# Kernel tuning notes

Measured on AMD Instinct MI355X. Metric: run time of the kernel, lower is better.

The kernel has to match this reference:

```python
import jax, jax.numpy as jnp
import numpy as np

N_NODES = 50000
N_EDGES = 800000
NFEAT, NHID, NCLASS, NCLUSTER = 512, 64, 16, 32


def gcn_conv(x, W, b, edge_index, edge_weight, n):
    """PyG GCNConv: add self-loops, symmetric normalization, linear + scatter-add."""
    row, col = edge_index[0], edge_index[1]
    loop = jnp.arange(n, dtype=row.dtype)
    row = jnp.concatenate([row, loop])
    col = jnp.concatenate([col, loop])
    w = jnp.concatenate([edge_weight, jnp.ones((n,), dtype=edge_weight.dtype)])
    # degree computed on target index (gcn_norm convention)
    deg = jax.ops.segment_sum(w, col, num_segments=n)
    dinv = jnp.where(deg > 0, jax.lax.rsqrt(deg), 0.0)
    norm = dinv[row] * w * dinv[col]          # [E+n]
    xw = x @ W                                # [n, out]
    msg = xw[row] * norm[:, None]             # gather + scale
    out = jax.ops.segment_sum(msg, col, num_segments=n)  # scatter-add
    return out + b


def setup_inputs() -> dict:
    key = jax.random.key(0)
    ks = jax.random.split(key, 12)
    def glorot(k, fan_in, fan_out):
        s = np.sqrt(6.0 / (fan_in + fan_out)).astype(np.float32)
        return jax.random.uniform(k, (fan_in, fan_out), jnp.float32, -s, s)
    x = jax.random.normal(ks[0], (N_NODES, NFEAT), jnp.float32)
    edge_index = jax.random.randint(ks[1], (2, N_EDGES), 0, N_NODES, dtype=jnp.int64)
    edge_weight = jax.random.uniform(ks[2], (N_EDGES,), jnp.float32)
    return {
        "x": x, "edge_index": edge_index, "edge_weight": edge_weight,
        "W1": glorot(ks[3], NFEAT, NHID), "b1": jnp.zeros((NHID,), jnp.float32),
        "W2": glorot(ks[4], NHID, NHID), "b2": jnp.zeros((NHID,), jnp.float32),
        "fcW1": glorot(ks[5], NHID, NCLASS), "fcb1": jnp.zeros((NCLASS,), jnp.float32),
        "fcW2": glorot(ks[6], NHID, NCLUSTER), "fcb2": jnp.zeros((NCLUSTER,), jnp.float32),
    }


def reference(x, edge_index, edge_weight, W1, b1, W2, b2, fcW1, fcb1, fcW2, fcb2):
    n = x.shape[0]
    h = jax.nn.relu(gcn_conv(x, W1, b1, edge_index, edge_weight, n))
    # dropout omitted (eval-mode / deterministic reference)
    h = gcn_conv(h, W2, b2, edge_index, edge_weight, n)
    pred = h @ fcW1 + fcb1
    pred_cluster = h @ fcW2 + fcb2
    return (pred, pred_cluster)
```

## Files before the change

### kernel.cpp

```cpp
#include <hip/hip_runtime.h>
#include <hip/hip_bf16.h>
#include <cstdint>
#include <cstddef>

#define N_FEAT 512
#define N_HID 64
#define N_CLASS 16
#define N_CLUSTER 32
#define NPART 8

typedef short short8 __attribute__((ext_vector_type(8)));
typedef float floatx4 __attribute__((ext_vector_type(4)));
typedef unsigned short u16;
typedef unsigned short u16x4 __attribute__((ext_vector_type(4)));

__device__ __forceinline__ short f2bf(float f) {
  __hip_bfloat16 h = __float2bfloat16(f);
  return *reinterpret_cast<short*>(&h);
}
__device__ __forceinline__ u16 f2bfu(float f) { return (u16)f2bf(f); }
__device__ __forceinline__ float bf2f(u16 u) {
  return __uint_as_float((unsigned)u << 16);
}

__device__ __forceinline__ void prepBF_one(const float* __restrict__ W,
                                           short* __restrict__ BF, int K, int idx) {
  int lane = idx & 63;
  int sj = idx >> 6;
  int j = sj & 3, s = sj >> 2;
  int col = j * 16 + (lane & 15);
  int k0 = s * 32 + ((lane >> 4) << 3);
  short8 v;
  #pragma unroll
  for (int t = 0; t < 8; ++t) v[t] = f2bf(W[(size_t)(k0 + t) * 64 + col]);
  *(short8*)(BF + (size_t)idx * 8) = v;
}

__global__ void k_init(uint4* __restrict__ h16, int n16,
                       const float* __restrict__ W1, short* __restrict__ BF1,
                       const float* __restrict__ W2, short* __restrict__ BF2,
                       int nbZ) {
  int b = blockIdx.x, t = threadIdx.x;
  if (b < nbZ) {
    int i = b * 256 + t;
    if (i < n16) h16[i] = make_uint4(0u, 0u, 0u, 0u);
  } else if (b < nbZ + 16) {
    prepBF_one(W1, BF1, N_FEAT, (b - nbZ) * 256 + t);
  } else {
    int idx = (b - nbZ - 16) * 256 + t;
    if (idx < 512) prepBF_one(W2, BF2, N_HID, idx);
  }
}

__global__ __launch_bounds__(256) void k_redscan(
    const unsigned long long* __restrict__ hist, int H,
    float* __restrict__ dinv, int* __restrict__ off,
    int* __restrict__ bsum, int n) {
  __shared__ int sh[256];
  int t = threadIdx.x;
  int i = blockIdx.x * 256 + t;
  int v = 0;
  if (i < n) {
    unsigned long long tot = 0;
    #pragma unroll
    for (int p = 0; p < NPART; ++p) tot += hist[(size_t)p * H + i];
    v = (int)(tot >> 40);
    float wsum = (float)(tot & ((1ull << 40) - 1)) * 5.9604644775390625e-08f;
    dinv[i] = rsqrtf(1.0f + wsum);
  }
  sh[t] = v;
  __syncthreads();
  #pragma unroll
  for (int d = 1; d < 256; d <<= 1) {
    int x = 0;
    if (t >= d) x = sh[t - d];
    __syncthreads();
    if (t >= d) sh[t] += x;
    __syncthreads();
  }
  if (i < n) off[i] = sh[t] - v;
  if (t == 255) bsum[blockIdx.x] = sh[255];
}

__global__ __launch_bounds__(256) void k_scan2(const int* __restrict__ bsum,
                                               int* __restrict__ bsum2, int nb) {
  __shared__ int sh[256];
  int t = threadIdx.x;
  int v = (t < nb) ? bsum[t] : 0;
  sh[t] = v;
  __syncthreads();
  #pragma unroll
  for (int d = 1; d < 256; d <<= 1) {
    int x = 0;
    if (t >= d) x = sh[t - d];
    __syncthreads();
    if (t >= d) sh[t] += x;
    __syncthreads();
  }
  if (t < nb) bsum2[t] = sh[t] - v;
}

__global__ void k_scan3_initcur(int* __restrict__ off, const int* __restrict__ bsum2,
                                const unsigned long long* __restrict__ hist, int H,
                                int* __restrict__ cur, int n, int E) {
  int i = blockIdx.x * 256 + threadIdx.x;
  if (i < n) {
    int o = off[i] + bsum2[blockIdx.x];
    off[i] = o;
    int running = o;
    #pragma unroll
    for (int p = 0; p < NPART; ++p) {
      cur[(size_t)p * H + i] = running;
      running += (int)(hist[(size_t)p * H + i] >> 40);
    }
  }
  if (i == 0) off[n] = E;
}

__device__ __forceinline__ void gemm_wave(
    const float* __restrict__ A, const short8* __restrict__ BF,
    u16* __restrict__ C, int M, int tile) {
  const int lane = threadIdx.x & 63;
  const int rbase = tile * 16;
  int r = rbase + (lane & 15);
  if (r >= M) r = M - 1;
  const float* arow = A + (size_t)r * 512 + ((lane >> 4) << 3);
  const short8* bbase = BF + lane;

  float4 pa0[4], pa1[4];
  short8 pb[2][4];
  #pragma unroll
  for (int s = 0; s < 4; ++s) {
    pa0[s] = *(const float4*)(arow + s * 32);
    pa1[s] = *(const float4*)(arow + s * 32 + 4);
  }
  #pragma unroll
  for (int s = 0; s < 2; ++s)
    #pragma unroll
    for (int j = 0; j < 4; ++j)
      pb[s][j] = bbase[(s * 4 + j) * 64];
  __builtin_amdgcn_sched_barrier(0);

  floatx4 acc[4];
  #pragma unroll
  for (int j = 0; j < 4; ++j) acc[j] = (floatx4){0.f, 0.f, 0.f, 0.f};

  #pragma unroll
  for (int s = 0; s < 16; ++s) {
    const int sa = s & 3;
    const int sb = s & 1;
    float4 a0 = pa0[sa], a1 = pa1[sa];
    short8 af;
    af[0] = f2bf(a0.x); af[1] = f2bf(a0.y); af[2] = f2bf(a0.z); af[3] = f2bf(a0.w);
    af[4] = f2bf(a1.x); af[5] = f2bf(a1.y); af[6] = f2bf(a1.z); af[7] = f2bf(a1.w);
    acc[0] = __builtin_amdgcn_mfma_f32_16x16x32_bf16(af, pb[sb][0], acc[0], 0, 0, 0);
    acc[1] = __builtin_amdgcn_mfma_f32_16x16x32_bf16(af, pb[sb][1], acc[1], 0, 0, 0);
    acc[2] = __builtin_amdgcn_mfma_f32_16x16x32_bf16(af, pb[sb][2], acc[2], 0, 0, 0);
    acc[3] = __builtin_amdgcn_mfma_f32_16x16x32_bf16(af, pb[sb][3], acc[3], 0, 0, 0);
    if (s + 4 < 16) {
      pa0[sa] = *(const float4*)(arow + (s + 4) * 32);
      pa1[sa] = *(const float4*)(arow + (s + 4) * 32 + 4);
    }
    if (s + 2 < 16) {
      #pragma unroll
      for (int j = 0; j < 4; ++j)
        pb[sb][j] = bbase[((s + 2) * 4 + j) * 64];
    }
    __builtin_amdgcn_sched_barrier(0);
  }

  const int srow = rbase + (lane >> 4) * 4;
  const int scol = lane & 15;
  #pragma unroll
  for (int i = 0; i < 4; ++i) {
    int rr = srow + i;
    if (rr < M) {
      #pragma unroll
      for (int j = 0; j < 4; ++j)
        C[(size_t)rr * 64 + j * 16 + scol] = f2bfu(acc[j][i]);
    }
  }
}

template<int MODE>
__global__ __launch_bounds__(256, 4) void k_fused(
    const float* __restrict__ A, const short8* __restrict__ BF,
    u16* __restrict__ C, int M, int nbT, int tile0, int S,
    const int* __restrict__ rowi, const int* __restrict__ coli,
    const float* __restrict__ w,
    unsigned long long* __restrict__ hist, int* __restrict__ rank,
    const float* __restrict__ dinv, const int* __restrict__ cur,
    unsigned* __restrict__ pairs, int H, int E) {
  const int q = blockIdx.x / (S + 1);
  const int r = blockIdx.x % (S + 1);
  if (r == 0) {
    int tile = tile0 + q * 4 + (threadIdx.x >> 6);
    if (tile < nbT) gemm_wave(A, BF, C, M, tile);
  } else {
    int f = q * S + (r - 1);
    int e = f * 256 + threadIdx.x;
    if (e >= E) return;
    int p = f & (NPART - 1);
    int c = coli[e];
    if constexpr (MODE == 0) {
      unsigned long long fx = (unsigned long long)__float2uint_rn(w[e] * 16777216.0f);
      unsigned long long old = atomicAdd(&hist[(size_t)p * H + c], (1ull << 40) | fx);
      rank[e] = (int)(old >> 40);
    } else {
      int rr = rowi[e];
      int pos = cur[(size_t)p * H + c] + rank[e];
      pairs[pos] = ((unsigned)rr << 16) | (u16)f2bf(dinv[rr] * w[e] * dinv[c]);
    }
  }
}

__global__ __launch_bounds__(64, 4) void k_mfma64(
    const u16* __restrict__ Av, const short8* __restrict__ BF,
    u16* __restrict__ C, int M) {
  const int lane = threadIdx.x & 63;
  const int rbase = blockIdx.x * 16;
  int r = rbase + (lane & 15);
  if (r >= M) r = M - 1;
  const int klo = (lane >> 4) * 8;
  const u16* arow = Av + (size_t)r * 64 + klo;
  const short8* bbase = BF + lane;

  short8 pah[2];
  short8 pb[2][4];
  pah[0] = *(const short8*)(arow);
  pah[1] = *(const short8*)(arow + 32);
  #pragma unroll
  for (int s = 0; s < 2; ++s)
    #pragma unroll
    for (int j = 0; j < 4; ++j)
      pb[s][j] = bbase[(s * 4 + j) * 64];

  floatx4 acc[4];
  #pragma unroll
  for (int j = 0; j < 4; ++j) acc[j] = (floatx4){0.f, 0.f, 0.f, 0.f};

  #pragma unroll
  for (int s = 0; s < 2; ++s) {
    acc[0] = __builtin_amdgcn_mfma_f32_16x16x32_bf16(pah[s], pb[s][0], acc[0], 0, 0, 0);
    acc[1] = __builtin_amdgcn_mfma_f32_16x16x32_bf16(pah[s], pb[s][1], acc[1], 0, 0, 0);
    acc[2] = __builtin_amdgcn_mfma_f32_16x16x32_bf16(pah[s], pb[s][2], acc[2], 0, 0, 0);
    acc[3] = __builtin_amdgcn_mfma_f32_16x16x32_bf16(pah[s], pb[s][3], acc[3], 0, 0, 0);
  }

  const int srow = rbase + (lane >> 4) * 4;
  const int scol = lane & 15;
  #pragma unroll
  for (int i = 0; i < 4; ++i) {
    int rr = srow + i;
    if (rr < M) {
      #pragma unroll
      for (int j = 0; j < 4; ++j)
        C[(size_t)rr * 64 + j * 16 + scol] = f2bfu(acc[j][i]);
    }
  }
}

template<bool RELU>
__global__ __launch_bounds__(256) void k_gather(
    const int* __restrict__ off, const unsigned* __restrict__ pairs,
    const float* __restrict__ dinv,
    const u16* __restrict__ xw, const float* __restrict__ bias,
    u16* __restrict__ h, int n) {
  int gid = blockIdx.x * 256 + threadIdx.x;
  int c = gid >> 6, lane = gid & 63;
  if (c >= n) return;
  float s = dinv[c]; s *= s;
  float acc = fmaf(bf2f(xw[(size_t)c * 64 + lane]), s, bias[lane]);
  int i = off[c], end = off[c + 1];
  for (; i + 7 < end; i += 8) {
    unsigned p[8];
    float v[8];
    #pragma unroll
    for (int t = 0; t < 8; ++t) p[t] = pairs[i + t];
    #pragma unroll
    for (int t = 0; t < 8; ++t)
      v[t] = bf2f(xw[(size_t)(p[t] >> 16) * 64 + lane]);
    #pragma unroll
    for (int t = 0; t < 8; ++t)
      acc = fmaf(v[t], __uint_as_float((p[t] & 0xffffu) << 16), acc);
  }
  for (; i + 1 < end; i += 2) {
    unsigned p0 = pairs[i], p1 = pairs[i + 1];
    float v0 = bf2f(xw[(size_t)(p0 >> 16) * 64 + lane]);
    float v1 = bf2f(xw[(size_t)(p1 >> 16) * 64 + lane]);
    acc = fmaf(v0, __uint_as_float((p0 & 0xffffu) << 16), acc);
    acc = fmaf(v1, __uint_as_float((p1 & 0xffffu) << 16), acc);
  }
  if (i < end) {
    unsigned p = pairs[i];
    acc = fmaf(bf2f(xw[(size_t)(p >> 16) * 64 + lane]),
               __uint_as_float((p & 0xffffu) << 16), acc);
  }
  if (RELU) acc = fmaxf(acc, 0.f);
  h[(size_t)c * 64 + lane] = f2bfu(acc);
}

__global__ __launch_bounds__(256) void k_fc(
    const u16* __restrict__ h,
    const float* __restrict__ fW1, const float* __restrict__ fb1,
    const float* __restrict__ fW2, const float* __restrict__ fb2,
    float* __restrict__ out, int M) {
  __shared__ float Hs[64][68];
  __shared__ float Ws[64][48];
  __shared__ float bs[48];
  const int t = threadIdx.x;
  const int row0 = blockIdx.x * 64;
  #pragma unroll
  for (int i = 0; i < 4; ++i) {
    int f = t + i * 256;
    int r = f >> 4, k4 = f & 15;
    int rr = row0 + r;
    float4 v = make_float4(0.f, 0.f, 0.f, 0.f);
    if (rr < M) {
      u16x4 u = *(const u16x4*)&h[(size_t)rr * 64 + k4 * 4];
      v = make_float4(bf2f(u[0]), bf2f(u[1]), bf2f(u[2]), bf2f(u[3]));
    }
    *(float4*)&Hs[r][k4 * 4] = v;
  }
  for (int f = t; f < 64 * 48; f += 256) {
    int k = f / 48, c = f - k * 48;
    Ws[k][c] = (c < 16) ? fW1[k * 16 + c] : fW2[k * 32 + (c - 16)];
  }
  if (t < 48) bs[t] = (t < 16) ? fb1[t] : fb2[t - 16];
  __syncthreads();
  const int tr = t >> 4, tc = t & 15;
  float acc[4][3] = {{0.f}};
  #pragma unroll 8
  for (int k = 0; k < 64; ++k) {
    float a[4], b[3];
    #pragma unroll
    for (int i = 0; i < 4; ++i) a[i] = Hs[tr * 4 + i][k];
    #pragma unroll
    for (int j = 0; j < 3; ++j) b[j] = Ws[k][tc * 3 + j];
    #pragma unroll
    for (int i = 0; i < 4; ++i)
      #pragma unroll
      for (int j = 0; j < 3; ++j) acc[i][j] = fmaf(a[i], b[j], acc[i][j]);
  }
  #pragma unroll
  for (int i = 0; i < 4; ++i) {
    int rr = row0 + tr * 4 + i;
    if (rr >= M) continue;
    #pragma unroll
    for (int j = 0; j < 3; ++j) {
      int c = tc * 3 + j;
      float v = acc[i][j] + bs[c];
      if (c < 16) out[(size_t)rr * 16 + c] = v;
      else out[(size_t)M * 16 + (size_t)rr * 32 + (c - 16)] = v;
    }
  }
}

extern "C" void kernel_launch(void* const* d_in, const int* in_sizes, int n_in,
                              void* d_out, int out_size, void* d_ws, size_t ws_size,
                              hipStream_t stream) {
  const float* x    = (const float*)d_in[0];
  const int*   ei   = (const int*)d_in[1];
  const float* ew   = (const float*)d_in[2];
  const float* W1   = (const float*)d_in[3];
  const float* b1   = (const float*)d_in[4];
  const float* W2   = (const float*)d_in[5];
  const float* b2   = (const float*)d_in[6];
  const float* fW1  = (const float*)d_in[7];
  const float* fb1  = (const float*)d_in[8];
  const float* fW2  = (const float*)d_in[9];
  const float* fb2  = (const float*)d_in[10];
  float* out = (float*)d_out;

  const int N = in_sizes[0] / N_FEAT;
  const int E = in_sizes[2];
  const int H = (N + 63) & ~63;
  const int* row = ei;
  const int* col = ei + E;

  char* ws = (char*)d_ws;
  float*              dinv = (float*)(ws + 0x000000);
  int*                off  = (int*)  (ws + 0x080000);
  int*                bsum = (int*)  (ws + 0x0C0000);
  int*                bsum2= (int*)  (ws + 0x0C1000);
  short*              BF1  = (short*)(ws + 0x0C8000);
  short*              BF2  = (short*)(ws + 0x0DA000);
  unsigned long long* hist = (unsigned long long*)(ws + 0x100000);
  int*                cur  = (int*)  (ws + 0x500000);
  unsigned*           pairs= (unsigned*)(ws + 0x6C0000);
  int*                rank = (int*)  (ws + 0xA00000);
  u16*                bufA = (u16*)  (ws + 0xD40000);
  u16*                bufB = (u16*)  (ws + 0x1980000);

  const int nbN  = (N + 255) / 256;
  const int nbE  = (E + 255) / 256;
  const int nbT  = (N + 15) / 16;
  const int nbG  = (N + 63) / 64;
  const int nbW  = (N * 64 + 255) / 256;
  const int nH16 = NPART * H / 2;
  const int nbZ  = (nH16 + 255) / 256;

  const int GA = 160;
  const int SA = (nbE + GA - 1) / GA;
  const int tilesA = GA * 4;
  const int GB = (nbT - tilesA + 3) / 4;
  const int SB = (nbE + GB - 1) / GB;

  k_init<<<nbZ + 18, 256, 0, stream>>>((uint4*)hist, nH16, W1, BF1, W2, BF2, nbZ);

  k_fused<0><<<GA * (SA + 1), 256, 0, stream>>>(
      x, (const short8*)BF1, bufA, N, nbT, 0, SA,
      row, col, ew, hist, rank, dinv, cur, pairs, H, E);

  k_redscan<<<nbN, 256, 0, stream>>>(hist, H, dinv, off, bsum, N);
  k_scan2  <<<1,   256, 0, stream>>>(bsum, bsum2, nbN);
  k_scan3_initcur<<<nbN, 256, 0, stream>>>(off, bsum2, hist, H, cur, N, E);

  k_fused<1><<<GB * (SB + 1), 256, 0, stream>>>(
      x, (const short8*)BF1, bufA, N, nbT, tilesA, SB,
      row, col, ew, hist, rank, dinv, cur, pairs, H, E);

  k_gather<true><<<nbW, 256, 0, stream>>>(off, pairs, dinv, bufA, b1, bufB, N);

  k_mfma64<<<nbT, 64, 0, stream>>>(bufB, (const short8*)BF2, bufA, N);
  k_gather<false><<<nbW, 256, 0, stream>>>(off, pairs, dinv, bufA, b2, bufB, N);

  k_fc<<<nbG, 256, 0, stream>>>(bufB, fW1, fb1, fW2, fb2, out, N);
}
```

Measured before the change: 186.0 us.

## Pre-convert x to bf16 alongside histogram pass, run full GEMM in second pass

```diff
diff --git a/kernel.cpp b/kernel.cpp
--- a/kernel.cpp
+++ b/kernel.cpp
@@ -13,6 +13,7 @@
 typedef float floatx4 __attribute__((ext_vector_type(4)));
 typedef unsigned short u16;
 typedef unsigned short u16x4 __attribute__((ext_vector_type(4)));
+typedef unsigned short u16x8 __attribute__((ext_vector_type(8)));
 
 __device__ __forceinline__ short f2bf(float f) {
   __hip_bfloat16 h = __float2bfloat16(f);
@@ -52,6 +53,34 @@
   }
 }
 
+__global__ __launch_bounds__(256, 4) void k_fusedA(
+    const float* __restrict__ x, u16* __restrict__ xbf, int nf8,
+    const int* __restrict__ coli, const float* __restrict__ w,
+    unsigned long long* __restrict__ hist, int* __restrict__ rank,
+    int H, int E, int nbE) {
+  const int q = blockIdx.x / 5;
+  const int r = blockIdx.x % 5;
+  if (r == 0) {
+    if (q >= nbE) return;
+    int e = q * 256 + threadIdx.x;
+    if (e >= E) return;
+    int p = q & (NPART - 1);
+    int c = coli[e];
+    unsigned long long fx = (unsigned long long)__float2uint_rn(w[e] * 16777216.0f);
+    unsigned long long old = atomicAdd(&hist[(size_t)p * H + c], (1ull << 40) | fx);
+    rank[e] = (int)(old >> 40);
+  } else {
+    int i = (q * 4 + (r - 1)) * 256 + threadIdx.x;
+    if (i >= nf8) return;
+    float4 a0 = *(const float4*)(x + (size_t)i * 8);
+    float4 a1 = *(const float4*)(x + (size_t)i * 8 + 4);
+    u16x8 o;
+    o[0] = f2bfu(a0.x); o[1] = f2bfu(a0.y); o[2] = f2bfu(a0.z); o[3] = f2bfu(a0.w);
+    o[4] = f2bfu(a1.x); o[5] = f2bfu(a1.y); o[6] = f2bfu(a1.z); o[7] = f2bfu(a1.w);
+    *(u16x8*)(xbf + (size_t)i * 8) = o;
+  }
+}
+
 __global__ __launch_bounds__(256) void k_redscan(
     const unsigned long long* __restrict__ hist, int H,
     float* __restrict__ dinv, int* __restrict__ off,
@@ -117,23 +146,21 @@
   if (i == 0) off[n] = E;
 }
 
-__device__ __forceinline__ void gemm_wave(
-    const float* __restrict__ A, const short8* __restrict__ BF,
+__device__ __forceinline__ void gemm_wave_bf(
+    const u16* __restrict__ A, const short8* __restrict__ BF,
     u16* __restrict__ C, int M, int tile) {
   const int lane = threadIdx.x & 63;
   const int rbase = tile * 16;
   int r = rbase + (lane & 15);
   if (r >= M) r = M - 1;
-  const float* arow = A + (size_t)r * 512 + ((lane >> 4) << 3);
+  const u16* arow = A + (size_t)r * 512 + ((lane >> 4) << 3);
   const short8* bbase = BF + lane;
 
-  float4 pa0[4], pa1[4];
+  short8 pa[4];
   short8 pb[2][4];
   #pragma unroll
-  for (int s = 0; s < 4; ++s) {
-    pa0[s] = *(const float4*)(arow + s * 32);
-    pa1[s] = *(const float4*)(arow + s * 32 + 4);
-  }
+  for (int s = 0; s < 4; ++s)
+    pa[s] = *(const short8*)(arow + s * 32);
   #pragma unroll
   for (int s = 0; s < 2; ++s)
     #pragma unroll
@@ -149,18 +176,13 @@
   for (int s = 0; s < 16; ++s) {
     const int sa = s & 3;
     const int sb = s & 1;
-    float4 a0 = pa0[sa], a1 = pa1[sa];
-    short8 af;
-    af[0] = f2bf(a0.x); af[1] = f2bf(a0.y); af[2] = f2bf(a0.z); af[3] = f2bf(a0.w);
-    af[4] = f2bf(a1.x); af[5] = f2bf(a1.y); af[6] = f2bf(a1.z); af[7] = f2bf(a1.w);
+    short8 af = pa[sa];
     acc[0] = __builtin_amdgcn_mfma_f32_16x16x32_bf16(af, pb[sb][0], acc[0], 0, 0, 0);
     acc[1] = __builtin_amdgcn_mfma_f32_16x16x32_bf16(af, pb[sb][1], acc[1], 0, 0, 0);
     acc[2] = __builtin_amdgcn_mfma_f32_16x16x32_bf16(af, pb[sb][2], acc[2], 0, 0, 0);
     acc[3] = __builtin_amdgcn_mfma_f32_16x16x32_bf16(af, pb[sb][3], acc[3], 0, 0, 0);
-    if (s + 4 < 16) {
-      pa0[sa] = *(const float4*)(arow + (s + 4) * 32);
-      pa1[sa] = *(const float4*)(arow + (s + 4) * 32 + 4);
-    }
+    if (s + 4 < 16)
+      pa[sa] = *(const short8*)(arow + (s + 4) * 32);
     if (s + 2 < 16) {
       #pragma unroll
       for (int j = 0; j < 4; ++j)
@@ -182,35 +204,28 @@
   }
 }
 
-template<int MODE>
-__global__ __launch_bounds__(256, 4) void k_fused(
-    const float* __restrict__ A, const short8* __restrict__ BF,
-    u16* __restrict__ C, int M, int nbT, int tile0, int S,
+__global__ __launch_bounds__(256, 4) void k_fusedB(
+    const u16* __restrict__ Abf, const short8* __restrict__ BF,
+    u16* __restrict__ C, int M, int nbT, int S,
     const int* __restrict__ rowi, const int* __restrict__ coli,
     const float* __restrict__ w,
-    unsigned long long* __restrict__ hist, int* __restrict__ rank,
-    const float* __restrict__ dinv, const int* __restrict__ cur,
-    unsigned* __restrict__ pairs, int H, int E) {
+    const int* __restrict__ rank, const float* __restrict__ dinv,
+    const int* __restrict__ cur, unsigned* __restrict__ pairs,
+    int H, int E) {
   const int q = blockIdx.x / (S + 1);
   const int r = blockIdx.x % (S + 1);
   if (r == 0) {
-    int tile = tile0 + q * 4 + (threadIdx.x >> 6);
-    if (tile < nbT) gemm_wave(A, BF, C, M, tile);
+    int tile = q * 4 + (threadIdx.x >> 6);
+    if (tile < nbT) gemm_wave_bf(Abf, BF, C, M, tile);
   } else {
     int f = q * S + (r - 1);
     int e = f * 256 + threadIdx.x;
     if (e >= E) return;
     int p = f & (NPART - 1);
     int c = coli[e];
-    if constexpr (MODE == 0) {
-      unsigned long long fx = (unsigned long long)__float2uint_rn(w[e] * 16777216.0f);
-      unsigned long long old = atomicAdd(&hist[(size_t)p * H + c], (1ull << 40) | fx);
-      rank[e] = (int)(old >> 40);
-    } else {
-      int rr = rowi[e];
-      int pos = cur[(size_t)p * H + c] + rank[e];
-      pairs[pos] = ((unsigned)rr << 16) | (u16)f2bf(dinv[rr] * w[e] * dinv[c]);
-    }
+    int rr = rowi[e];
+    int pos = cur[(size_t)p * H + c] + rank[e];
+    pairs[pos] = ((unsigned)rr << 16) | (u16)f2bf(dinv[rr] * w[e] * dinv[c]);
   }
 }
 
@@ -391,6 +406,7 @@
   int*                rank = (int*)  (ws + 0xA00000);
   u16*                bufA = (u16*)  (ws + 0xD40000);
   u16*                bufB = (u16*)  (ws + 0x1980000);
+  u16*                xbf  = (u16*)  (ws + 0x2400000);
 
   const int nbN  = (N + 255) / 256;
   const int nbE  = (E + 255) / 256;
@@ -399,26 +415,24 @@
   const int nbW  = (N * 64 + 255) / 256;
   const int nH16 = NPART * H / 2;
   const int nbZ  = (nH16 + 255) / 256;
-
-  const int GA = 160;
-  const int SA = (nbE + GA - 1) / GA;
-  const int tilesA = GA * 4;
-  const int GB = (nbT - tilesA + 3) / 4;
+  const int nf8  = N * N_FEAT / 8;
+  const int ncv  = (nf8 + 255) / 256;
+
+  const int QA = (nbE > (ncv + 3) / 4) ? nbE : (ncv + 3) / 4;
+  const int GB = (nbT + 3) / 4;
   const int SB = (nbE + GB - 1) / GB;
 
   k_init<<<nbZ + 18, 256, 0, stream>>>((uint4*)hist, nH16, W1, BF1, W2, BF2, nbZ);
 
-  k_fused<0><<<GA * (SA + 1), 256, 0, stream>>>(
-      x, (const short8*)BF1, bufA, N, nbT, 0, SA,
-      row, col, ew, hist, rank, dinv, cur, pairs, H, E);
+  k_fusedA<<<QA * 5, 256, 0, stream>>>(x, xbf, nf8, col, ew, hist, rank, H, E, nbE);
 
   k_redscan<<<nbN, 256, 0, stream>>>(hist, H, dinv, off, bsum, N);
   k_scan2  <<<1,   256, 0, stream>>>(bsum, bsum2, nbN);
   k_scan3_initcur<<<nbN, 256, 0, stream>>>(off, bsum2, hist, H, cur, N, E);
 
-  k_fused<1><<<GB * (SB + 1), 256, 0, stream>>>(
-      x, (const short8*)BF1, bufA, N, nbT, tilesA, SB,
-      row, col, ew, hist, rank, dinv, cur, pairs, H, E);
+  k_fusedB<<<GB * (SB + 1), 256, 0, stream>>>(
+      xbf, (const short8*)BF1, bufA, N, nbT, SB,
+      row, col, ew, rank, dinv, cur, pairs, H, E);
 
   k_gather<true><<<nbW, 256, 0, stream>>>(off, pairs, dinv, bufA, b1, bufB, N);
 
```

Result: faster. 172.7 us (-7.2%).
